# Optimization experiments

Measured on AMD Instinct MI355X. Metric: run time of the kernel, lower is better.

## Reference

```python
import jax, jax.numpy as jnp
import numpy as np

BATCH_SIZE = 4096
D = 128
TEMPERATURE = 0.5
EPS = 1e-8  # torch CosineSimilarity eps


def _neg_indices(batch_size):
    # flat indices of the (N, N-2) negative entries: all but diagonal and the +/-B pair
    N = 2 * batch_size
    mask = np.ones((N, N), dtype=bool)
    np.fill_diagonal(mask, False)
    i = np.arange(batch_size)
    mask[i, batch_size + i] = False
    mask[batch_size + i, i] = False
    return np.where(mask.ravel())[0]


NEG_IDX = jnp.asarray(_neg_indices(BATCH_SIZE))


def setup_inputs() -> dict:
    key = jax.random.key(0)
    k1, k2 = jax.random.split(key)
    return {
        "z_i": jax.random.normal(k1, (BATCH_SIZE, D), dtype=jnp.float32),
        "z_j": jax.random.normal(k2, (BATCH_SIZE, D), dtype=jnp.float32),
    }


def reference(z_i, z_j):
    batch_size = z_i.shape[0]
    N = 2 * batch_size
    z = jnp.concatenate([z_i, z_j], axis=0)                       # [N, D]
    norm = jnp.maximum(jnp.linalg.norm(z, axis=1, keepdims=True), EPS)
    zn = z / norm
    sim = (zn @ zn.T) / TEMPERATURE                               # [N, N] cosine sim / temp
    # positives: diagonals at offset +/- batch_size
    pos = jnp.concatenate(
        [jnp.diagonal(sim, offset=batch_size), jnp.diagonal(sim, offset=-batch_size)],
        axis=0,
    )                                                             # [N]
    neg = sim.ravel()[NEG_IDX].reshape(N, N - 2)                  # masked gather
    logits = jnp.concatenate([pos[:, None], neg], axis=1)         # [N, N-1], label = 0
    # CrossEntropyLoss(reduction='sum') with labels all 0, then / N
    loss = jnp.sum(jax.nn.logsumexp(logits, axis=1) - logits[:, 0]) / N
    return loss
```

## Files before the change

### kernel.cpp

```cpp
#include <hip/hip_runtime.h>
#include <hip/hip_bf16.h>
#include <type_traits>


#define BATCH 4096
#define N_TOT 8192
#define DIM 128
#define ROWS_PER_WAVE 32
#define WAVES_PER_BLK 4
#define GRP 128
#define NGRP 64
#define NPAIR ((NGRP * (NGRP + 1)) / 2)
#define TILE_C 64
#define NROWBLK 32

#define C_LOG2E2 2.8853900817779268f

using bf16x8 = __attribute__((ext_vector_type(8))) __bf16;
using f32x4  = __attribute__((ext_vector_type(4))) float;

typedef __attribute__((address_space(1))) const void cg_void;
typedef __attribute__((address_space(3))) void lds_void;
__device__ __forceinline__ void gll16(const void* g, void* l) {
    __builtin_amdgcn_global_load_lds((cg_void*)g, (lds_void*)l, 16, 0, 0);
}

__global__ __launch_bounds__(256) void k_normalize(const float* __restrict__ zi,
                                                   const float* __restrict__ zj,
                                                   __hip_bfloat16* __restrict__ zn) {
    int row  = blockIdx.x * 4 + (threadIdx.x >> 6);
    int lane = threadIdx.x & 63;
    const float* src = (row < BATCH) ? (zi + (size_t)row * DIM)
                                     : (zj + (size_t)(row - BATCH) * DIM);
    float2 v = ((const float2*)src)[lane];
    float ss = v.x * v.x + v.y * v.y;
    #pragma unroll
    for (int m = 1; m < 64; m <<= 1) ss += __shfl_xor(ss, m);
    float inv = 1.0f / fmaxf(sqrtf(ss), 1e-8f);
    __hip_bfloat162 o;
    o.x = __float2bfloat16(v.x * inv);
    o.y = __float2bfloat16(v.y * inv);
    ((__hip_bfloat162*)(zn + (size_t)row * DIM))[lane] = o;
}

__global__ __launch_bounds__(256, 4) void k_main(const __hip_bfloat16* __restrict__ zn_,
                                                 float* __restrict__ S_contrib) {
    __shared__ __align__(16) char Bs[2][TILE_C * 256];
    __shared__ float colred[WAVES_PER_BLK][GRP];

    const int tid  = threadIdx.x;
    const int lane = tid & 63;
    const int wv   = tid >> 6;
    const int l15  = lane & 15;
    const int lb   = lane >> 4;

    int I = 0, rem = blockIdx.x;
    while (rem >= NGRP - I) { rem -= NGRP - I; ++I; }
    const int J = I + rem;
    const bool isdiag = (I == J);

    const int wr0 = I * GRP + wv * ROWS_PER_WAVE;
    const int cs0 = J * GRP;

    const __bf16* zn = (const __bf16*)zn_;

    bf16x8 a_[2][4];
    #pragma unroll
    for (int g = 0; g < 2; ++g) {
        const __bf16* p = zn + (size_t)(wr0 + g * 16 + l15) * DIM + lb * 8;
        #pragma unroll
        for (int s = 0; s < 4; ++s)
            a_[g][s] = *(const bf16x8*)(p + s * 32);
    }

    const char* gB = (const char*)(zn + (size_t)cs0 * DIM);
    int srcoff[4];
    #pragma unroll
    for (int i = 0; i < 4; ++i) {
        int m = (wv * 4 + i) * 64 + lane;
        int c = m >> 4, slot = m & 15;
        int j = slot ^ (c & 7);
        srcoff[i] = c * 256 + j * 16;
    }

    #pragma unroll
    for (int t = 0; t < 2; ++t) {
        const char* src = gB + (size_t)t * (TILE_C * 256);
        #pragma unroll
        for (int i = 0; i < 4; ++i)
            gll16(src + srcoff[i], Bs[t] + (wv * 4 + i) * 1024);
    }

    f32x4 sumexp[2] = {};
    float csr[8] = {};

    __syncthreads();

    auto COMPUTE = [&](auto tc) {
        constexpr int t = tc.value;
        const char* buf = Bs[t];
        const int c0t = cs0 + t * TILE_C;
        const bool diagtile = ((unsigned)(wr0 - c0t) < (unsigned)TILE_C);
        #pragma unroll
        for (int cb = 0; cb < 4; ++cb) {
            const int c = cb * 16 + l15;
            const char* pc = buf + c * 256;
            bf16x8 b[4];
            #pragma unroll
            for (int s = 0; s < 4; ++s)
                b[s] = *(const bf16x8*)(pc + ((lb + s * 4) ^ (c & 7)) * 16);
            f32x4 acc[2] = {};
            #pragma unroll
            for (int g = 0; g < 2; ++g)
                #pragma unroll
                for (int s = 0; s < 4; ++s)
                    acc[g] = __builtin_amdgcn_mfma_f32_16x16x32_bf16(a_[g][s], b[s], acc[g], 0, 0, 0);
            const int mycol = c0t + c;
            if (diagtile) {
                #pragma unroll
                for (int g = 0; g < 2; ++g)
                    #pragma unroll
                    for (int v = 0; v < 4; ++v) {
                        float e = __builtin_amdgcn_exp2f(acc[g][v] * C_LOG2E2);
                        int row = wr0 + g * 16 + lb * 4 + v;
                        sumexp[g][v] += (mycol == row) ? 0.0f : e;
                    }
            } else {
                float cs = 0.0f;
                #pragma unroll
                for (int g = 0; g < 2; ++g)
                    #pragma unroll
                    for (int v = 0; v < 4; ++v) {
                        float e = __builtin_amdgcn_exp2f(acc[g][v] * C_LOG2E2);
                        sumexp[g][v] += e;
                        cs += e;
                    }
                csr[t * 4 + cb] += cs;
            }
        }
    };

    COMPUTE(std::integral_constant<int, 0>{});
    COMPUTE(std::integral_constant<int, 1>{});

    #pragma unroll
    for (int m = 1; m <= 8; m <<= 1)
        #pragma unroll
        for (int g = 0; g < 2; ++g)
            #pragma unroll
            for (int v = 0; v < 4; ++v)
                sumexp[g][v] += __shfl_xor(sumexp[g][v], m);

    if (l15 == 0) {
        #pragma unroll
        for (int g = 0; g < 2; ++g) {
            int row = wr0 + g * 16 + lb * 4;
            *(f32x4*)&S_contrib[(size_t)J * N_TOT + row] = sumexp[g];
        }
    }

    if (!isdiag) {
        #pragma unroll
        for (int k = 0; k < 8; ++k) {
            float v = csr[k];
            v += __shfl_xor(v, 16);
            v += __shfl_xor(v, 32);
            if (lb == 0) colred[wv][k * 16 + l15] = v;
        }
        __syncthreads();
        if (tid < GRP) {
            float s = colred[0][tid] + colred[1][tid] + colred[2][tid] + colred[3][tid];
            S_contrib[(size_t)I * N_TOT + cs0 + tid] = s;
        }
    }
}

__device__ inline float bdot(unsigned a, unsigned b) {
    float alo = __uint_as_float(a << 16), ahi = __uint_as_float(a & 0xffff0000u);
    float blo = __uint_as_float(b << 16), bhi = __uint_as_float(b & 0xffff0000u);
    return fmaf(alo, blo, ahi * bhi);
}

__global__ __launch_bounds__(256) void k_rowsum(const float* __restrict__ S_contrib,
                                                const __hip_bfloat16* __restrict__ zn_,
                                                float* __restrict__ blk_out) {
    const int r = blockIdx.x * 256 + threadIdx.x;
    float S = 0.0f;
    #pragma unroll
    for (int s = 0; s < NGRP; ++s) S += S_contrib[(size_t)s * N_TOT + r];

    const uint4* pa = (const uint4*)((const __bf16*)zn_ + (size_t)r * DIM);
    const uint4* pb = (const uint4*)((const __bf16*)zn_ + (size_t)(r ^ BATCH) * DIM);
    float dot = 0.0f;
    #pragma unroll
    for (int c = 0; c < DIM / 8; ++c) {
        uint4 ua = pa[c], ub = pb[c];
        dot += bdot(ua.x, ub.x) + bdot(ua.y, ub.y) + bdot(ua.z, ub.z) + bdot(ua.w, ub.w);
    }

    float contrib = __logf(S) - 2.0f * dot;

    #pragma unroll
    for (int m = 1; m < 64; m <<= 1) contrib += __shfl_xor(contrib, m);
    __shared__ float sm[4];
    if ((threadIdx.x & 63) == 0) sm[threadIdx.x >> 6] = contrib;
    __syncthreads();
    if (threadIdx.x == 0) blk_out[blockIdx.x] = sm[0] + sm[1] + sm[2] + sm[3];
}

__global__ void k_final(const float* __restrict__ blk_out, float* __restrict__ out) {
    float v = (threadIdx.x < NROWBLK) ? blk_out[threadIdx.x] : 0.0f;
    #pragma unroll
    for (int m = 1; m < 64; m <<= 1) v += __shfl_xor(v, m);
    if (threadIdx.x == 0) out[0] = v / (float)N_TOT;
}

extern "C" void kernel_launch(void* const* d_in, const int* in_sizes, int n_in,
                              void* d_out, int out_size, void* d_ws, size_t ws_size,
                              hipStream_t stream) {
    const float* zi = (const float*)d_in[0];
    const float* zj = (const float*)d_in[1];
    char* ws = (char*)d_ws;
    __hip_bfloat16* zn = (__hip_bfloat16*)ws;
    float* S_contrib = (float*)(ws + (size_t)2 * 1024 * 1024);
    float* blk       = (float*)(ws + (size_t)4 * 1024 * 1024);
    float* out       = (float*)d_out;

    k_normalize<<<N_TOT / 4, 256, 0, stream>>>(zi, zj, zn);
    k_main<<<NPAIR, 256, 0, stream>>>(zn, S_contrib);
    k_rowsum<<<NROWBLK, 256, 0, stream>>>(S_contrib, zn, blk);
    k_final<<<1, 64, 0, stream>>>(blk, out);
}
```

Before: 37.55 us.

## Process two column groups per block with double-buffered staging in symmetric sim kernel

Each block now covers a 128-row group against two adjacent 128-column groups (1024 such blocks plus 32 single-group blocks), instead of one pair per block. The A fragments are reused across twice as many columns, and B tiles are double-buffered so the next tile's load overlaps the current compute. The partial-sum layout is reorganised into row-chunk and column-chunk regions, and the row-sum kernel is adjusted to match. The aim is to cut block count, A reload overhead and scheduling imbalance, at the cost of more complex index mapping and extra barriers.

```diff
diff --git a/kernel.cpp b/kernel.cpp
--- a/kernel.cpp
+++ b/kernel.cpp
@@ -6,13 +6,11 @@
 #define BATCH 4096
 #define N_TOT 8192
 #define DIM 128
-#define ROWS_PER_WAVE 32
-#define WAVES_PER_BLK 4
 #define GRP 128
 #define NGRP 64
-#define NPAIR ((NGRP * (NGRP + 1)) / 2)
 #define TILE_C 64
-#define NROWBLK 32
+#define NBLK 1056
+#define NSLOT 96
 
 #define C_LOG2E2 2.8853900817779268f
 
@@ -46,7 +44,7 @@
 __global__ __launch_bounds__(256, 4) void k_main(const __hip_bfloat16* __restrict__ zn_,
                                                  float* __restrict__ S_contrib) {
     __shared__ __align__(16) char Bs[2][TILE_C * 256];
-    __shared__ float colred[WAVES_PER_BLK][GRP];
+    __shared__ float colred[4][256];
 
     const int tid  = threadIdx.x;
     const int lane = tid & 63;
@@ -54,13 +52,25 @@
     const int l15  = lane & 15;
     const int lb   = lane >> 4;
 
-    int I = 0, rem = blockIdx.x;
-    while (rem >= NGRP - I) { rem -= NGRP - I; ++I; }
-    const int J = I + rem;
-    const bool isdiag = (I == J);
-
-    const int wr0 = I * GRP + wv * ROWS_PER_WAVE;
-    const int cs0 = J * GRP;
+    int I, c, ngrp2;
+    if (blockIdx.x < 1024) {
+        const int fbid = blockIdx.x;
+        int m = (int)(32.0f - sqrtf((float)(1024 - fbid)));
+        while ((m + 1) * (63 - m) <= fbid) ++m;
+        while (m * (64 - m) > fbid) --m;
+        int rem = fbid - m * (64 - m);
+        int h = 32 - m;
+        I = 2 * m + (rem >= h ? 1 : 0);
+        c = rem - (rem >= h ? h : 0);
+        ngrp2 = 2;
+    } else {
+        const int hbid = blockIdx.x - 1024;
+        I = 2 * hbid + 1;
+        c = 31 - hbid;
+        ngrp2 = 1;
+    }
+    const int J0  = I + 2 * c;
+    const int wr0 = I * GRP + wv * 32;
 
     const __bf16* zn = (const __bf16*)zn_;
 
@@ -73,49 +83,47 @@
             a_[g][s] = *(const bf16x8*)(p + s * 32);
     }
 
-    const char* gB = (const char*)(zn + (size_t)cs0 * DIM);
+    const char* gB = (const char*)(zn + (size_t)J0 * GRP * DIM);
     int srcoff[4];
     #pragma unroll
     for (int i = 0; i < 4; ++i) {
-        int m = (wv * 4 + i) * 64 + lane;
-        int c = m >> 4, slot = m & 15;
-        int j = slot ^ (c & 7);
-        srcoff[i] = c * 256 + j * 16;
-    }
-
-    #pragma unroll
-    for (int t = 0; t < 2; ++t) {
+        int m2 = (wv * 4 + i) * 64 + lane;
+        int col = m2 >> 4, slot = m2 & 15;
+        srcoff[i] = col * 256 + (slot ^ (col & 7)) * 16;
+    }
+
+    auto STAGE = [&](int t) {
         const char* src = gB + (size_t)t * (TILE_C * 256);
         #pragma unroll
         for (int i = 0; i < 4; ++i)
-            gll16(src + srcoff[i], Bs[t] + (wv * 4 + i) * 1024);
-    }
+            gll16(src + srcoff[i], Bs[t & 1] + (wv * 4 + i) * 1024);
+    };
 
     f32x4 sumexp[2] = {};
-    float csr[8] = {};
-
-    __syncthreads();
-
-    auto COMPUTE = [&](auto tc) {
+    float csr[16] = {};
+
+    auto CMP = [&](auto tc) {
         constexpr int t = tc.value;
-        const char* buf = Bs[t];
-        const int c0t = cs0 + t * TILE_C;
+        const char* buf = Bs[t & 1];
+        const int c0t = J0 * GRP + t * TILE_C;
+        const int Jg  = J0 + (t >> 1);
         const bool diagtile = ((unsigned)(wr0 - c0t) < (unsigned)TILE_C);
+        const bool docol    = (Jg != I);
         #pragma unroll
         for (int cb = 0; cb < 4; ++cb) {
-            const int c = cb * 16 + l15;
-            const char* pc = buf + c * 256;
+            const int cc = cb * 16 + l15;
+            const char* pc = buf + cc * 256;
             bf16x8 b[4];
             #pragma unroll
             for (int s = 0; s < 4; ++s)
-                b[s] = *(const bf16x8*)(pc + ((lb + s * 4) ^ (c & 7)) * 16);
+                b[s] = *(const bf16x8*)(pc + ((lb + s * 4) ^ (cc & 7)) * 16);
             f32x4 acc[2] = {};
             #pragma unroll
             for (int g = 0; g < 2; ++g)
                 #pragma unroll
                 for (int s = 0; s < 4; ++s)
                     acc[g] = __builtin_amdgcn_mfma_f32_16x16x32_bf16(a_[g][s], b[s], acc[g], 0, 0, 0);
-            const int mycol = c0t + c;
+            const int mycol = c0t + cc;
             if (diagtile) {
                 #pragma unroll
                 for (int g = 0; g < 2; ++g)
@@ -135,13 +143,23 @@
                         sumexp[g][v] += e;
                         cs += e;
                     }
-                csr[t * 4 + cb] += cs;
+                if (docol) csr[t * 4 + cb] += cs;
             }
         }
     };
 
-    COMPUTE(std::integral_constant<int, 0>{});
-    COMPUTE(std::integral_constant<int, 1>{});
+    STAGE(0);
+    if (ngrp2 == 2) {
+        __syncthreads(); STAGE(1);
+        CMP(std::integral_constant<int, 0>{}); __syncthreads(); STAGE(2);
+        CMP(std::integral_constant<int, 1>{}); __syncthreads(); STAGE(3);
+        CMP(std::integral_constant<int, 2>{}); __syncthreads();
+        CMP(std::integral_constant<int, 3>{});
+    } else {
+        STAGE(1); __syncthreads();
+        CMP(std::integral_constant<int, 0>{});
+        CMP(std::integral_constant<int, 1>{});
+    }
 
     #pragma unroll
     for (int m = 1; m <= 8; m <<= 1)
@@ -155,22 +173,23 @@
         #pragma unroll
         for (int g = 0; g < 2; ++g) {
             int row = wr0 + g * 16 + lb * 4;
-            *(f32x4*)&S_contrib[(size_t)J * N_TOT + row] = sumexp[g];
+            *(f32x4*)&S_contrib[(size_t)c * N_TOT + row] = sumexp[g];
         }
     }
 
-    if (!isdiag) {
-        #pragma unroll
-        for (int k = 0; k < 8; ++k) {
-            float v = csr[k];
-            v += __shfl_xor(v, 16);
-            v += __shfl_xor(v, 32);
-            if (lb == 0) colred[wv][k * 16 + l15] = v;
-        }
-        __syncthreads();
-        if (tid < GRP) {
+    #pragma unroll
+    for (int k = 0; k < 16; ++k) {
+        float v = csr[k];
+        v += __shfl_xor(v, 16);
+        v += __shfl_xor(v, 32);
+        if (lb == 0) colred[wv][k * 16 + l15] = v;
+    }
+    __syncthreads();
+    if (tid < GRP * ngrp2) {
+        int Jg = J0 + (tid >> 7);
+        if (Jg != I) {
             float s = colred[0][tid] + colred[1][tid] + colred[2][tid] + colred[3][tid];
-            S_contrib[(size_t)I * N_TOT + cs0 + tid] = s;
+            S_contrib[(size_t)(32 + I) * N_TOT + J0 * GRP + tid] = s;
         }
     }
 }
@@ -181,20 +200,23 @@
     return fmaf(alo, blo, ahi * bhi);
 }
 
-__global__ __launch_bounds__(256) void k_rowsum(const float* __restrict__ S_contrib,
+__global__ __launch_bounds__(128) void k_rowsum(const float* __restrict__ S_contrib,
                                                 const __hip_bfloat16* __restrict__ zn_,
                                                 float* __restrict__ blk_out) {
-    const int r = blockIdx.x * 256 + threadIdx.x;
+    const int G = blockIdx.x;
+    const int r = G * GRP + threadIdx.x;
+    const int nch = (65 - G) >> 1;
+
     float S = 0.0f;
-    #pragma unroll
-    for (int s = 0; s < NGRP; ++s) S += S_contrib[(size_t)s * N_TOT + r];
+    for (int s = 0; s < nch; ++s)      S += S_contrib[(size_t)s * N_TOT + r];
+    for (int s = 32; s < 32 + G; ++s)  S += S_contrib[(size_t)s * N_TOT + r];
 
     const uint4* pa = (const uint4*)((const __bf16*)zn_ + (size_t)r * DIM);
     const uint4* pb = (const uint4*)((const __bf16*)zn_ + (size_t)(r ^ BATCH) * DIM);
     float dot = 0.0f;
     #pragma unroll
-    for (int c = 0; c < DIM / 8; ++c) {
-        uint4 ua = pa[c], ub = pb[c];
+    for (int cc = 0; cc < DIM / 8; ++cc) {
+        uint4 ua = pa[cc], ub = pb[cc];
         dot += bdot(ua.x, ub.x) + bdot(ua.y, ub.y) + bdot(ua.z, ub.z) + bdot(ua.w, ub.w);
     }
 
@@ -202,14 +224,14 @@
 
     #pragma unroll
     for (int m = 1; m < 64; m <<= 1) contrib += __shfl_xor(contrib, m);
-    __shared__ float sm[4];
+    __shared__ float sm[2];
     if ((threadIdx.x & 63) == 0) sm[threadIdx.x >> 6] = contrib;
     __syncthreads();
-    if (threadIdx.x == 0) blk_out[blockIdx.x] = sm[0] + sm[1] + sm[2] + sm[3];
+    if (threadIdx.x == 0) blk_out[G] = sm[0] + sm[1];
 }
 
 __global__ void k_final(const float* __restrict__ blk_out, float* __restrict__ out) {
-    float v = (threadIdx.x < NROWBLK) ? blk_out[threadIdx.x] : 0.0f;
+    float v = blk_out[threadIdx.x];
     #pragma unroll
     for (int m = 1; m < 64; m <<= 1) v += __shfl_xor(v, m);
     if (threadIdx.x == 0) out[0] = v / (float)N_TOT;
@@ -223,11 +245,11 @@
     char* ws = (char*)d_ws;
     __hip_bfloat16* zn = (__hip_bfloat16*)ws;
     float* S_contrib = (float*)(ws + (size_t)2 * 1024 * 1024);
-    float* blk       = (float*)(ws + (size_t)4 * 1024 * 1024);
+    float* blk       = (float*)(ws + (size_t)5 * 1024 * 1024 + 65536);
     float* out       = (float*)d_out;
 
     k_normalize<<<N_TOT / 4, 256, 0, stream>>>(zi, zj, zn);
-    k_main<<<NPAIR, 256, 0, stream>>>(zn, S_contrib);
-    k_rowsum<<<NROWBLK, 256, 0, stream>>>(S_contrib, zn, blk);
+    k_main<<<NBLK, 256, 0, stream>>>(zn, S_contrib);
+    k_rowsum<<<NGRP, 128, 0, stream>>>(S_contrib, zn, blk);
     k_final<<<1, 64, 0, stream>>>(blk, out);
 }
```

After: 66.89 us. 1.78x slower.
